# Kernel optimization log

Hardware: AMD Instinct MI355X
Metric: run time of the kernel (lower is better)

Reference implementation:

```python
import math
import jax, jax.numpy as jnp
import numpy as np

S, B, D, H = 2048, 2, 1024, 16
DK = D // H

def setup_inputs() -> dict:
    key = jax.random.key(0)
    ks = jax.random.split(key, 11)
    std = 1.0 / math.sqrt(D)
    inp = {
        "query": jax.random.normal(ks[0], (S, B, D), jnp.float32),
        "key": jax.random.normal(ks[1], (S, B, D), jnp.float32),
        "value": jax.random.normal(ks[2], (S, B, D), jnp.float32),
        "mask": jnp.ones((1, S, 1), dtype=bool),
        "Wq": jax.random.normal(ks[3], (D, D), jnp.float32) * std,
        "bq": jnp.zeros((D,), jnp.float32),
        "Wk": jax.random.normal(ks[4], (D, D), jnp.float32) * std,
        "bk": jnp.zeros((D,), jnp.float32),
        "Wv": jax.random.normal(ks[5], (D, D), jnp.float32) * std,
        "bv": jnp.zeros((D,), jnp.float32),
        "Wo": jax.random.normal(ks[6], (D, D), jnp.float32) * std,
        "bo": jnp.zeros((D,), jnp.float32),
    }
    return inp


def reference(query, key, value, mask, Wq, bq, Wk, bk, Wv, bv, Wo, bo):
    scale = 1.0 / math.sqrt(DK)
    # project and split heads: [S, B, D] -> [S, B, H, DK]
    q = (query @ Wq.T + bq).reshape(S, B, H, DK)
    k = (key @ Wk.T + bk).reshape(S, B, H, DK)
    v = (value @ Wv.T + bv).reshape(S, B, H, DK)
    # scores: [S_q, S_k, B, H]
    scores = jnp.einsum('ibhd,jbhd->ijbh', q, k) * scale
    m = mask[..., None]  # [1, S_k, 1, 1] broadcast over i, b, h
    scores = jnp.where(m, scores, jnp.float32(-jnp.inf))
    attn = jax.nn.softmax(scores, axis=1)  # softmax over key axis j
    # dropout is eval-mode identity
    x = jnp.einsum('ijbh,jbhd->ibhd', attn, v).reshape(S, B, D)
    return x @ Wo.T + bo
```

## Files before the change

kernel.cpp:

```cpp
#include <hip/hip_runtime.h>
#include <hip/hip_bf16.h>
#include <stdint.h>

typedef __bf16 bf16;
typedef __bf16 bf16x4 __attribute__((ext_vector_type(4)));
typedef __bf16 bf16x8 __attribute__((ext_vector_type(8)));
typedef float  f32x4  __attribute__((ext_vector_type(4)));


static __device__ __forceinline__ void load_lds16(const bf16* g, bf16* l) {
    __builtin_amdgcn_global_load_lds(
        (__attribute__((address_space(1))) void*)(g),
        (__attribute__((address_space(3))) void*)(l), 16, 0, 0);
}

#define WAIT_LGKM0  asm volatile("s_waitcnt lgkmcnt(0)" ::: "memory")
#define BARRIER_PIN() do { __builtin_amdgcn_s_barrier(); \
                           __builtin_amdgcn_sched_barrier(0); } while (0)

static __device__ __forceinline__ int swz64(int row, int col) {
    return row * 64 + (col ^ ((row & 7) << 3));
}
static __device__ __forceinline__ int swz32(int row, int col) {
    return row * 32 + (col ^ (((row >> 1) & 3) << 3));
}

__global__ __launch_bounds__(256) void cast_w(
    const float* __restrict__ W0, const float* __restrict__ W1,
    const float* __restrict__ W2, const float* __restrict__ W3,
    bf16* __restrict__ out)
{
    const int sel = blockIdx.y;
    const float* W = sel == 0 ? W0 : (sel == 1 ? W1 : (sel == 2 ? W2 : W3));
    const size_t base = ((size_t)blockIdx.x * 256 + threadIdx.x) * 8;
    float4 a = *(const float4*)(W + base);
    float4 b = *(const float4*)(W + base + 4);
    bf16x8 v = { (bf16)a.x,(bf16)a.y,(bf16)a.z,(bf16)a.w,
                 (bf16)b.x,(bf16)b.y,(bf16)b.z,(bf16)b.w };
    *(bf16x8*)(out + (size_t)sel * 1024 * 1024 + base) = v;
}

__global__ __launch_bounds__(256, 8) void gemm_qkv(
    const float* __restrict__ Aq, const float* __restrict__ Ak, const float* __restrict__ Av,
    const bf16* __restrict__ Wb,
    const float* __restrict__ bq, const float* __restrict__ bk, const float* __restrict__ bv,
    bf16* __restrict__ Oq, bf16* __restrict__ Ok, bf16* __restrict__ Ov)
{
    __shared__ __align__(16) bf16 smem[8192];

    const int tid  = threadIdx.x;
    const int wave = tid >> 6, lane = tid & 63;
    const int m0  = blockIdx.x * 64;
    const int sel = blockIdx.y >> 4;
    const int n0  = (blockIdx.y & 15) * 64;
    const float* A    = sel == 0 ? Aq : (sel == 1 ? Ak : Av);
    const bf16*  W    = Wb + (size_t)sel * 1024 * 1024;
    const float* bias = sel == 0 ? bq : (sel == 1 ? bk : bv);
    bf16*        O    = sel == 0 ? Oq : (sel == 1 ? Ok : Ov);

    const int wm = (wave & 1) * 32, wn = (wave >> 1) * 32;
    const int fm = lane & 15, fq = lane >> 4;
    const int srow = tid >> 2, sc8 = (tid & 3) * 8;
    const int ldr = lane >> 2;
    const int ldc = ((lane & 3) ^ ((ldr >> 1) & 3)) * 8;
    const int K = 1024;
    const int fsw = (fq ^ ((fm >> 1) & 3)) * 8;

    bf16* Asb = smem;
    bf16* Wsb = smem + 4096;
    const float* Ald = A + (size_t)(m0 + srow) * K + sc8;
    const bf16*  Wld = W + (size_t)(n0 + wave * 16 + ldr) * K + ldc;
    const int    wofs = wave * 16 * 32;

    f32x4 acc[2][2];
    #pragma unroll
    for (int i = 0; i < 2; i++)
        #pragma unroll
        for (int t = 0; t < 2; t++) acc[i][t] = f32x4{0.f, 0.f, 0.f, 0.f};

    float4 a0 = *(const float4*)(Ald);
    float4 a1 = *(const float4*)(Ald + 4);
    load_lds16(Wld, Wsb + wofs);
    {
        bf16x8 va = { (bf16)a0.x,(bf16)a0.y,(bf16)a0.z,(bf16)a0.w,
                      (bf16)a1.x,(bf16)a1.y,(bf16)a1.z,(bf16)a1.w };
        *(bf16x8*)(Asb + swz32(srow, sc8)) = va;
    }
    __syncthreads();

    for (int t = 0; t < 32; t++) {
        const int cur = t & 1;
        if (t < 31) {
            const int k1 = (t + 1) * 32;
            a0 = *(const float4*)(Ald + k1);
            a1 = *(const float4*)(Ald + k1 + 4);
            load_lds16(Wld + k1, Wsb + (cur ^ 1) * 2048 + wofs);
        }
        const bf16* Asc = Asb + cur * 2048;
        const bf16* Wsc = Wsb + cur * 2048;
        bf16x8 af[2], bw[2];
        #pragma unroll
        for (int i = 0; i < 2; i++)
            af[i] = *(const bf16x8*)(Asc + (wm + i * 16 + fm) * 32 + fsw);
        #pragma unroll
        for (int t4 = 0; t4 < 2; t4++)
            bw[t4] = *(const bf16x8*)(Wsc + (wn + t4 * 16 + fm) * 32 + fsw);
        #pragma unroll
        for (int i = 0; i < 2; i++)
            #pragma unroll
            for (int t4 = 0; t4 < 2; t4++)
                acc[i][t4] = __builtin_amdgcn_mfma_f32_16x16x32_bf16(
                    af[i], bw[t4], acc[i][t4], 0, 0, 0);
        if (t < 31) {
            bf16x8 va = { (bf16)a0.x,(bf16)a0.y,(bf16)a0.z,(bf16)a0.w,
                          (bf16)a1.x,(bf16)a1.y,(bf16)a1.z,(bf16)a1.w };
            *(bf16x8*)(Asb + (cur ^ 1) * 2048 + swz32(srow, sc8)) = va;
        }
        __syncthreads();
    }

    if (sel == 2) {
        constexpr int TP = 40;
        bf16* Tr = smem;
        const int ecol = tid >> 2, es8 = (tid & 3) * 8;
        #pragma unroll
        for (int p = 0; p < 2; p++) {
            __syncthreads();
            #pragma unroll
            for (int tt = 0; tt < 2; tt++) {
                const int lcol = wn + tt * 16 + fm;
                const float bvv = bias[n0 + lcol];
                #pragma unroll
                for (int i = 0; i < 2; i++) {
                    const int lrow = wm + i * 16 + fq * 4;
                    #pragma unroll
                    for (int rh = 0; rh < 2; rh++) {
                        const int r = p + rh * 2;
                        Tr[lcol * TP + ((lrow + r) >> 1)] = (bf16)(acc[i][tt][r] + bvv);
                    }
                }
            }
            __syncthreads();
            const size_t gb = (size_t)(n0 + ecol) * 2048
                            + (size_t)p * 2097152 + (m0 >> 1) + es8;
            *(bf16x8*)(O + gb) = *(const bf16x8*)(Tr + ecol * TP + es8);
        }
    } else {
        #pragma unroll
        for (int tt = 0; tt < 2; tt++) {
            const int col = n0 + wn + tt * 16 + fm;
            const float bvv = bias[col];
            #pragma unroll
            for (int i = 0; i < 2; i++) {
                const int rbase = m0 + wm + i * 16 + fq * 4;
                #pragma unroll
                for (int r = 0; r < 4; r++)
                    O[(size_t)(rbase + r) * 1024 + col] = (bf16)(acc[i][tt][r] + bvv);
            }
        }
    }
}

__global__ __launch_bounds__(256, 8) void gemm_out(
    const bf16* __restrict__ A, const bf16* __restrict__ W,
    const float* __restrict__ bias, float* __restrict__ C)
{
    __shared__ __align__(16) bf16 smem[8192];

    const int tid  = threadIdx.x;
    const int wave = tid >> 6, lane = tid & 63;
    const int m0 = blockIdx.x * 64;
    const int n0 = blockIdx.y * 64;
    const int wm = (wave & 1) * 32, wn = (wave >> 1) * 32;
    const int fm = lane & 15, fq = lane >> 4;
    const int ldr = lane >> 2;
    const int ldc = ((lane & 3) ^ ((ldr >> 1) & 3)) * 8;
    const int K = 1024;
    const int fsw = (fq ^ ((fm >> 1) & 3)) * 8;

    bf16* Asb = smem;
    bf16* Wsb = smem + 4096;
    const bf16* Ald = A + (size_t)(m0 + wave * 16 + ldr) * K + ldc;
    const bf16* Wld = W + (size_t)(n0 + wave * 16 + ldr) * K + ldc;
    const int   wofs = wave * 16 * 32;

    f32x4 acc[2][2];
    #pragma unroll
    for (int i = 0; i < 2; i++)
        #pragma unroll
        for (int t = 0; t < 2; t++) acc[i][t] = f32x4{0.f, 0.f, 0.f, 0.f};

    load_lds16(Ald, Asb + wofs);
    load_lds16(Wld, Wsb + wofs);
    __syncthreads();

    for (int t = 0; t < 32; t++) {
        const int cur = t & 1;
        if (t < 31) {
            const int k1 = (t + 1) * 32;
            load_lds16(Ald + k1, Asb + (cur ^ 1) * 2048 + wofs);
            load_lds16(Wld + k1, Wsb + (cur ^ 1) * 2048 + wofs);
        }
        const bf16* Asc = Asb + cur * 2048;
        const bf16* Wsc = Wsb + cur * 2048;
        bf16x8 af[2], bw[2];
        #pragma unroll
        for (int i = 0; i < 2; i++)
            af[i] = *(const bf16x8*)(Asc + (wm + i * 16 + fm) * 32 + fsw);
        #pragma unroll
        for (int t4 = 0; t4 < 2; t4++)
            bw[t4] = *(const bf16x8*)(Wsc + (wn + t4 * 16 + fm) * 32 + fsw);
        #pragma unroll
        for (int i = 0; i < 2; i++)
            #pragma unroll
            for (int t4 = 0; t4 < 2; t4++)
                acc[i][t4] = __builtin_amdgcn_mfma_f32_16x16x32_bf16(
                    af[i], bw[t4], acc[i][t4], 0, 0, 0);
        __syncthreads();
    }

    #pragma unroll
    for (int t = 0; t < 2; t++) {
        const int col = n0 + wn + t * 16 + fm;
        const float bvv = bias[col];
        #pragma unroll
        for (int i = 0; i < 2; i++) {
            const int rbase = m0 + wm + i * 16 + fq * 4;
            #pragma unroll
            for (int r = 0; r < 4; r++)
                C[(size_t)(rbase + r) * 1024 + col] = acc[i][t][r] + bvv;
        }
    }
}

__global__ __launch_bounds__(256) void attn_fused(
    const bf16* __restrict__ Qp, const bf16* __restrict__ Kp,
    const bf16* __restrict__ VTp, bf16* __restrict__ Xp)
{
    __shared__ __align__(16) bf16 Ks[64 * 64];
    __shared__ __align__(16) bf16 Vt[64 * 64];
    __shared__ __align__(16) bf16 SP[64 * 64];

    const int qt = blockIdx.x, h = blockIdx.y, b = blockIdx.z;
    const int tid  = threadIdx.x;
    const int wave = tid >> 6, lane = tid & 63;
    const int fm = lane & 15, fq = lane >> 4;
    const size_t off = (size_t)b * 1024 + h * 64;
    const size_t vrow0 = ((size_t)b * 16 + h) * 64;
    const int s0 = qt * 64;
    const int sr  = tid >> 3;
    const int scc = (tid & 7) * 8;

    for (int c = tid; c < 512; c += 256) {
        const int r = c >> 3, cc = (c & 7) * 8;
        *(bf16x8*)(SP + swz64(r, cc)) =
            *(const bf16x8*)(Qp + (size_t)(s0 + r) * 2048 + off + cc);
    }
    __syncthreads();
    bf16x8 aq[2];
    #pragma unroll
    for (int ks = 0; ks < 2; ks++) {
        aq[ks] = *(const bf16x8*)(SP + swz64(wave * 16 + fm, ks * 32 + fq * 8));
        #pragma unroll
        for (int j = 0; j < 8; j++)
            aq[ks][j] = (bf16)((float)aq[ks][j] * 0.125f);
    }

    f32x4 o[4];
    #pragma unroll
    for (int dt = 0; dt < 4; dt++) o[dt] = f32x4{0.f, 0.f, 0.f, 0.f};
    float lsum = 0.f;
    bf16* Pw = SP + wave * 16 * 64;

    bf16x8 kp0 = *(const bf16x8*)(Kp  + (size_t)(sr) * 2048 + off + scc);
    bf16x8 kp1 = *(const bf16x8*)(Kp  + (size_t)(32 + sr) * 2048 + off + scc);
    bf16x8 vp0 = *(const bf16x8*)(VTp + (vrow0 + sr) * 2048 + scc);
    bf16x8 vp1 = *(const bf16x8*)(VTp + (vrow0 + 32 + sr) * 2048 + scc);

    for (int kt = 0; kt < 32; kt++) {
        WAIT_LGKM0;
        BARRIER_PIN();
        *(bf16x8*)(Ks + swz64(sr, scc))      = kp0;
        *(bf16x8*)(Ks + swz64(32 + sr, scc)) = kp1;
        *(bf16x8*)(Vt + swz64(sr, scc))      = vp0;
        *(bf16x8*)(Vt + swz64(32 + sr, scc)) = vp1;
        if (kt < 31) {
            const int kn = (kt + 1) * 64;
            kp0 = *(const bf16x8*)(Kp  + (size_t)(kn + sr) * 2048 + off + scc);
            kp1 = *(const bf16x8*)(Kp  + (size_t)(kn + 32 + sr) * 2048 + off + scc);
            vp0 = *(const bf16x8*)(VTp + (vrow0 + sr) * 2048 + kn + scc);
            vp1 = *(const bf16x8*)(VTp + (vrow0 + 32 + sr) * 2048 + kn + scc);
        }
        WAIT_LGKM0;
        BARRIER_PIN();

        f32x4 sf[4];
        #pragma unroll
        for (int t = 0; t < 4; t++) sf[t] = f32x4{0.f, 0.f, 0.f, 0.f};
        __builtin_amdgcn_s_setprio(1);
        #pragma unroll
        for (int ks = 0; ks < 2; ks++)
            #pragma unroll
            for (int t = 0; t < 4; t++) {
                bf16x8 bk_ = *(const bf16x8*)(Ks + swz64(t * 16 + fm, ks * 32 + fq * 8));
                sf[t] = __builtin_amdgcn_mfma_f32_16x16x32_bf16(bk_, aq[ks], sf[t], 0, 0, 0);
            }
        __builtin_amdgcn_s_setprio(0);

        #pragma unroll
        for (int t = 0; t < 4; t++) {
            const float p0 = __expf(sf[t][0]);
            const float p1 = __expf(sf[t][1]);
            const float p2 = __expf(sf[t][2]);
            const float p3 = __expf(sf[t][3]);
            lsum += (p0 + p1) + (p2 + p3);
            bf16x4 pk = { (bf16)p0, (bf16)p1, (bf16)p2, (bf16)p3 };
            *(bf16x4*)(Pw + swz64(fm, t * 16 + fq * 4)) = pk;
        }

        __builtin_amdgcn_s_setprio(1);
        #pragma unroll
        for (int ks = 0; ks < 2; ks++) {
            bf16x8 ap = *(const bf16x8*)(Pw + swz64(fm, ks * 32 + fq * 8));
            #pragma unroll
            for (int dt = 0; dt < 4; dt++) {
                bf16x8 bv_ = *(const bf16x8*)(Vt + swz64(dt * 16 + fm, ks * 32 + fq * 8));
                o[dt] = __builtin_amdgcn_mfma_f32_16x16x32_bf16(ap, bv_, o[dt], 0, 0, 0);
            }
        }
        __builtin_amdgcn_s_setprio(0);
    }

    float l = lsum;
    l += __shfl_xor(l, 16);
    l += __shfl_xor(l, 32);
    float linv[4];
    #pragma unroll
    for (int r = 0; r < 4; r++)
        linv[r] = 1.f / __shfl(l, fq * 4 + r);
    #pragma unroll
    for (int dt = 0; dt < 4; dt++) {
        const int d = dt * 16 + fm;
        #pragma unroll
        for (int r = 0; r < 4; r++) {
            const int s = s0 + wave * 16 + fq * 4 + r;
            Xp[(size_t)s * 2048 + off + d] = (bf16)(o[dt][r] * linv[r]);
        }
    }
}

extern "C" void kernel_launch(void* const* d_in, const int* in_sizes, int n_in,
                              void* d_out, int out_size, void* d_ws, size_t ws_size,
                              hipStream_t stream) {
    const float* qkv[3]; const float* Wm[4]; const float* bm[4];
    int nq = 0, nw = 0, nb = 0;
    for (int i = 0; i < n_in; i++) {
        const int sz = in_sizes[i];
        if (sz == 4 * 1024 * 1024 && nq < 3)      qkv[nq++] = (const float*)d_in[i];
        else if (sz == 1024 * 1024 && nw < 4)     Wm[nw++]  = (const float*)d_in[i];
        else if (sz == 1024 && nb < 4)            bm[nb++]  = (const float*)d_in[i];
    }

    bf16* Wb = (bf16*)d_ws;
    bf16* q  = Wb + (size_t)4 * 1024 * 1024;
    bf16* k  = q  + (size_t)4096 * 1024;
    bf16* v  = k  + (size_t)4096 * 1024;
    bf16* x  = q;

    cast_w<<<dim3(512, 4), 256, 0, stream>>>(Wm[0], Wm[1], Wm[2], Wm[3], Wb);
    gemm_qkv<<<dim3(64, 48), 256, 0, stream>>>(
        qkv[0], qkv[1], qkv[2], Wb, bm[0], bm[1], bm[2], q, k, v);
    attn_fused<<<dim3(32, 16, 2), 256, 0, stream>>>(q, k, v, x);
    gemm_out<<<dim3(64, 16), 256, 0, stream>>>(
        x, Wb + (size_t)3 * 1024 * 1024, bm[3], (float*)d_out);
}
```

Baseline: 249.9 us.

## Fuse fp32 weight casting into GEMM loaders and widen QKV tile to 64x128

Drops the separate cast_w kernel. The QKV and output GEMMs now load fp32 weights directly, convert them to bf16 in registers and store them into swizzled LDS, which removes a launch and the write/read round trip of the bf16 weight copy. The QKV GEMM tile grows from 64x64 to 64x128 so each A tile is reused across more columns, at the cost of more LDS, more registers and lower occupancy (launch bound 6). The weights are now read as fp32 by every block, which doubles weight traffic per block, and the output GEMM gives up the async LDS load for its weight operand.

```diff
diff --git a/kernel.cpp b/kernel.cpp
--- a/kernel.cpp
+++ b/kernel.cpp
@@ -25,96 +25,88 @@
     return row * 32 + (col ^ (((row >> 1) & 3) << 3));
 }
 
-__global__ __launch_bounds__(256) void cast_w(
-    const float* __restrict__ W0, const float* __restrict__ W1,
-    const float* __restrict__ W2, const float* __restrict__ W3,
-    bf16* __restrict__ out)
-{
-    const int sel = blockIdx.y;
-    const float* W = sel == 0 ? W0 : (sel == 1 ? W1 : (sel == 2 ? W2 : W3));
-    const size_t base = ((size_t)blockIdx.x * 256 + threadIdx.x) * 8;
-    float4 a = *(const float4*)(W + base);
-    float4 b = *(const float4*)(W + base + 4);
+static __device__ __forceinline__ void store8(bf16* dst, float4 a, float4 b) {
     bf16x8 v = { (bf16)a.x,(bf16)a.y,(bf16)a.z,(bf16)a.w,
                  (bf16)b.x,(bf16)b.y,(bf16)b.z,(bf16)b.w };
-    *(bf16x8*)(out + (size_t)sel * 1024 * 1024 + base) = v;
-}
-
-__global__ __launch_bounds__(256, 8) void gemm_qkv(
+    *(bf16x8*)dst = v;
+}
+
+__global__ __launch_bounds__(256, 6) void gemm_qkv(
     const float* __restrict__ Aq, const float* __restrict__ Ak, const float* __restrict__ Av,
-    const bf16* __restrict__ Wb,
+    const float* __restrict__ Wq, const float* __restrict__ Wk, const float* __restrict__ Wv,
     const float* __restrict__ bq, const float* __restrict__ bk, const float* __restrict__ bv,
     bf16* __restrict__ Oq, bf16* __restrict__ Ok, bf16* __restrict__ Ov)
 {
-    __shared__ __align__(16) bf16 smem[8192];
+    __shared__ __align__(16) bf16 smem[12288];
 
     const int tid  = threadIdx.x;
     const int wave = tid >> 6, lane = tid & 63;
     const int m0  = blockIdx.x * 64;
-    const int sel = blockIdx.y >> 4;
-    const int n0  = (blockIdx.y & 15) * 64;
+    const int sel = blockIdx.y >> 3;
+    const int n0  = (blockIdx.y & 7) * 128;
     const float* A    = sel == 0 ? Aq : (sel == 1 ? Ak : Av);
-    const bf16*  W    = Wb + (size_t)sel * 1024 * 1024;
+    const float* Wf   = sel == 0 ? Wq : (sel == 1 ? Wk : Wv);
     const float* bias = sel == 0 ? bq : (sel == 1 ? bk : bv);
     bf16*        O    = sel == 0 ? Oq : (sel == 1 ? Ok : Ov);
 
-    const int wm = (wave & 1) * 32, wn = (wave >> 1) * 32;
+    const int wm = (wave & 1) * 32, wn = (wave >> 1) * 64;
     const int fm = lane & 15, fq = lane >> 4;
     const int srow = tid >> 2, sc8 = (tid & 3) * 8;
-    const int ldr = lane >> 2;
-    const int ldc = ((lane & 3) ^ ((ldr >> 1) & 3)) * 8;
     const int K = 1024;
     const int fsw = (fq ^ ((fm >> 1) & 3)) * 8;
 
     bf16* Asb = smem;
     bf16* Wsb = smem + 4096;
-    const float* Ald = A + (size_t)(m0 + srow) * K + sc8;
-    const bf16*  Wld = W + (size_t)(n0 + wave * 16 + ldr) * K + ldc;
-    const int    wofs = wave * 16 * 32;
-
-    f32x4 acc[2][2];
+    const float* Ald = A  + (size_t)(m0 + srow) * K + sc8;
+    const float* Wld = Wf + (size_t)(n0 + srow) * K + sc8;
+
+    f32x4 acc[2][4];
     #pragma unroll
     for (int i = 0; i < 2; i++)
         #pragma unroll
-        for (int t = 0; t < 2; t++) acc[i][t] = f32x4{0.f, 0.f, 0.f, 0.f};
-
-    float4 a0 = *(const float4*)(Ald);
-    float4 a1 = *(const float4*)(Ald + 4);
-    load_lds16(Wld, Wsb + wofs);
-    {
-        bf16x8 va = { (bf16)a0.x,(bf16)a0.y,(bf16)a0.z,(bf16)a0.w,
-                      (bf16)a1.x,(bf16)a1.y,(bf16)a1.z,(bf16)a1.w };
-        *(bf16x8*)(Asb + swz32(srow, sc8)) = va;
-    }
+        for (int t = 0; t < 4; t++) acc[i][t] = f32x4{0.f, 0.f, 0.f, 0.f};
+
+    float4 a0  = *(const float4*)(Ald);
+    float4 a1  = *(const float4*)(Ald + 4);
+    float4 w0a = *(const float4*)(Wld);
+    float4 w0b = *(const float4*)(Wld + 4);
+    float4 w1a = *(const float4*)(Wld + (size_t)64 * K);
+    float4 w1b = *(const float4*)(Wld + (size_t)64 * K + 4);
+    store8(Asb + swz32(srow, sc8), a0, a1);
+    store8(Wsb + swz32(srow, sc8), w0a, w0b);
+    store8(Wsb + swz32(64 + srow, sc8), w1a, w1b);
     __syncthreads();
 
     for (int t = 0; t < 32; t++) {
         const int cur = t & 1;
         if (t < 31) {
             const int k1 = (t + 1) * 32;
-            a0 = *(const float4*)(Ald + k1);
-            a1 = *(const float4*)(Ald + k1 + 4);
-            load_lds16(Wld + k1, Wsb + (cur ^ 1) * 2048 + wofs);
+            a0  = *(const float4*)(Ald + k1);
+            a1  = *(const float4*)(Ald + k1 + 4);
+            w0a = *(const float4*)(Wld + k1);
+            w0b = *(const float4*)(Wld + k1 + 4);
+            w1a = *(const float4*)(Wld + (size_t)64 * K + k1);
+            w1b = *(const float4*)(Wld + (size_t)64 * K + k1 + 4);
         }
         const bf16* Asc = Asb + cur * 2048;
-        const bf16* Wsc = Wsb + cur * 2048;
-        bf16x8 af[2], bw[2];
+        const bf16* Wsc = Wsb + cur * 4096;
+        bf16x8 af[2], bw[4];
         #pragma unroll
         for (int i = 0; i < 2; i++)
             af[i] = *(const bf16x8*)(Asc + (wm + i * 16 + fm) * 32 + fsw);
         #pragma unroll
-        for (int t4 = 0; t4 < 2; t4++)
+        for (int t4 = 0; t4 < 4; t4++)
             bw[t4] = *(const bf16x8*)(Wsc + (wn + t4 * 16 + fm) * 32 + fsw);
         #pragma unroll
         for (int i = 0; i < 2; i++)
             #pragma unroll
-            for (int t4 = 0; t4 < 2; t4++)
+            for (int t4 = 0; t4 < 4; t4++)
                 acc[i][t4] = __builtin_amdgcn_mfma_f32_16x16x32_bf16(
                     af[i], bw[t4], acc[i][t4], 0, 0, 0);
         if (t < 31) {
-            bf16x8 va = { (bf16)a0.x,(bf16)a0.y,(bf16)a0.z,(bf16)a0.w,
-                          (bf16)a1.x,(bf16)a1.y,(bf16)a1.z,(bf16)a1.w };
-            *(bf16x8*)(Asb + (cur ^ 1) * 2048 + swz32(srow, sc8)) = va;
+            store8(Asb + (cur ^ 1) * 2048 + swz32(srow, sc8), a0, a1);
+            store8(Wsb + (cur ^ 1) * 4096 + swz32(srow, sc8), w0a, w0b);
+            store8(Wsb + (cur ^ 1) * 4096 + swz32(64 + srow, sc8), w1a, w1b);
         }
         __syncthreads();
     }
@@ -122,12 +114,13 @@
     if (sel == 2) {
         constexpr int TP = 40;
         bf16* Tr = smem;
-        const int ecol = tid >> 2, es8 = (tid & 3) * 8;
+        const int ecol = tid & 127;
+        const int esh  = (tid >> 7) * 16;
         #pragma unroll
         for (int p = 0; p < 2; p++) {
             __syncthreads();
             #pragma unroll
-            for (int tt = 0; tt < 2; tt++) {
+            for (int tt = 0; tt < 4; tt++) {
                 const int lcol = wn + tt * 16 + fm;
                 const float bvv = bias[n0 + lcol];
                 #pragma unroll
@@ -142,12 +135,15 @@
             }
             __syncthreads();
             const size_t gb = (size_t)(n0 + ecol) * 2048
-                            + (size_t)p * 2097152 + (m0 >> 1) + es8;
-            *(bf16x8*)(O + gb) = *(const bf16x8*)(Tr + ecol * TP + es8);
+                            + (size_t)p * 2097152 + (m0 >> 1) + esh;
+            bf16x8 v0 = *(const bf16x8*)(Tr + ecol * TP + esh);
+            bf16x8 v1 = *(const bf16x8*)(Tr + ecol * TP + esh + 8);
+            *(bf16x8*)(O + gb)     = v0;
+            *(bf16x8*)(O + gb + 8) = v1;
         }
     } else {
         #pragma unroll
-        for (int tt = 0; tt < 2; tt++) {
+        for (int tt = 0; tt < 4; tt++) {
             const int col = n0 + wn + tt * 16 + fm;
             const float bvv = bias[col];
             #pragma unroll
@@ -162,7 +158,7 @@
 }
 
 __global__ __launch_bounds__(256, 8) void gemm_out(
-    const bf16* __restrict__ A, const bf16* __restrict__ W,
+    const bf16* __restrict__ A, const float* __restrict__ Wf,
     const float* __restrict__ bias, float* __restrict__ C)
 {
     __shared__ __align__(16) bf16 smem[8192];
@@ -175,14 +171,15 @@
     const int fm = lane & 15, fq = lane >> 4;
     const int ldr = lane >> 2;
     const int ldc = ((lane & 3) ^ ((ldr >> 1) & 3)) * 8;
+    const int srow = tid >> 2, sc8 = (tid & 3) * 8;
     const int K = 1024;
     const int fsw = (fq ^ ((fm >> 1) & 3)) * 8;
 
     bf16* Asb = smem;
     bf16* Wsb = smem + 4096;
-    const bf16* Ald = A + (size_t)(m0 + wave * 16 + ldr) * K + ldc;
-    const bf16* Wld = W + (size_t)(n0 + wave * 16 + ldr) * K + ldc;
-    const int   wofs = wave * 16 * 32;
+    const bf16*  Ald = A  + (size_t)(m0 + wave * 16 + ldr) * K + ldc;
+    const float* Wld = Wf + (size_t)(n0 + srow) * K + sc8;
+    const int    aofs = wave * 16 * 32;
 
     f32x4 acc[2][2];
     #pragma unroll
@@ -190,16 +187,19 @@
         #pragma unroll
         for (int t = 0; t < 2; t++) acc[i][t] = f32x4{0.f, 0.f, 0.f, 0.f};
 
-    load_lds16(Ald, Asb + wofs);
-    load_lds16(Wld, Wsb + wofs);
+    load_lds16(Ald, Asb + aofs);
+    float4 w0a = *(const float4*)(Wld);
+    float4 w0b = *(const float4*)(Wld + 4);
+    store8(Wsb + swz32(srow, sc8), w0a, w0b);
     __syncthreads();
 
     for (int t = 0; t < 32; t++) {
         const int cur = t & 1;
         if (t < 31) {
             const int k1 = (t + 1) * 32;
-            load_lds16(Ald + k1, Asb + (cur ^ 1) * 2048 + wofs);
-            load_lds16(Wld + k1, Wsb + (cur ^ 1) * 2048 + wofs);
+            load_lds16(Ald + k1, Asb + (cur ^ 1) * 2048 + aofs);
+            w0a = *(const float4*)(Wld + k1);
+            w0b = *(const float4*)(Wld + k1 + 4);
         }
         const bf16* Asc = Asb + cur * 2048;
         const bf16* Wsc = Wsb + cur * 2048;
@@ -216,6 +216,8 @@
             for (int t4 = 0; t4 < 2; t4++)
                 acc[i][t4] = __builtin_amdgcn_mfma_f32_16x16x32_bf16(
                     af[i], bw[t4], acc[i][t4], 0, 0, 0);
+        if (t < 31)
+            store8(Wsb + (cur ^ 1) * 2048 + swz32(srow, sc8), w0a, w0b);
         __syncthreads();
     }
 
@@ -361,16 +363,15 @@
         else if (sz == 1024 && nb < 4)            bm[nb++]  = (const float*)d_in[i];
     }
 
-    bf16* Wb = (bf16*)d_ws;
-    bf16* q  = Wb + (size_t)4 * 1024 * 1024;
-    bf16* k  = q  + (size_t)4096 * 1024;
-    bf16* v  = k  + (size_t)4096 * 1024;
+    bf16* q  = (bf16*)d_ws;
+    bf16* k  = q + (size_t)4096 * 1024;
+    bf16* v  = k + (size_t)4096 * 1024;
     bf16* x  = q;
 
-    cast_w<<<dim3(512, 4), 256, 0, stream>>>(Wm[0], Wm[1], Wm[2], Wm[3], Wb);
-    gemm_qkv<<<dim3(64, 48), 256, 0, stream>>>(
-        qkv[0], qkv[1], qkv[2], Wb, bm[0], bm[1], bm[2], q, k, v);
+    gemm_qkv<<<dim3(64, 24), 256, 0, stream>>>(
+        qkv[0], qkv[1], qkv[2], Wm[0], Wm[1], Wm[2],
+        bm[0], bm[1], bm[2], q, k, v);
     attn_fused<<<dim3(32, 16, 2), 256, 0, stream>>>(q, k, v, x);
     gemm_out<<<dim3(64, 16), 256, 0, stream>>>(
-        x, Wb + (size_t)3 * 1024 * 1024, bm[3], (float*)d_out);
-}
+        x, Wm[3], bm[3], (float*)d_out);
+}
```

Result: slower. 261.6 us (+4.7%).
